# Kernel optimization log

Hardware: AMD Instinct MI355X
Metric: run time of the kernel (lower is better)

## Reference

```python
import jax, jax.numpy as jnp
import numpy as np

NUM_HEADS = 16
HEAD_DIM = 64


def setup_inputs() -> dict:
    key = jax.random.key(0)
    k1, k2, k3 = jax.random.split(key, 3)
    B, N, D = 4, 2048, NUM_HEADS * HEAD_DIM
    q = jax.random.normal(k1, (B, N, D), dtype=jnp.float32)
    k = jax.random.normal(k2, (B, N, D), dtype=jnp.float32)
    v = jax.random.normal(k3, (B, N, D), dtype=jnp.float32)
    # causal mask: True where attention is allowed
    attn_mask = jnp.tril(jnp.ones((N, N), dtype=bool))
    return {"q": q, "k": k, "v": v, "attn_mask": attn_mask}


def reference(q, k, v, attn_mask):
    B, N, D = q.shape
    H, Hd = NUM_HEADS, HEAD_DIM
    # [B, N, H*Hd] -> [B, H, N, Hd]
    qh = q.reshape(B, N, H, Hd).transpose(0, 2, 1, 3)
    kh = k.reshape(B, N, H, Hd).transpose(0, 2, 1, 3)
    vh = v.reshape(B, N, H, Hd).transpose(0, 2, 1, 3)
    scale = 1.0 / jnp.sqrt(jnp.asarray(Hd, dtype=q.dtype))
    scores = jnp.einsum('bhqd,bhkd->bhqk', qh, kh) * scale  # [B,H,N,N]
    scores = jnp.where(attn_mask[None, None, :, :], scores, -jnp.inf)
    probs = jax.nn.softmax(scores, axis=-1)
    y = jnp.einsum('bhqk,bhkd->bhqd', probs, vh)  # [B,H,N,Hd]
    return y.transpose(0, 2, 1, 3).reshape(B, N, H * Hd)
```

## Files before the change

### kernel.cpp

```cpp
#include <hip/hip_runtime.h>

#define RS 1024
#define SEQLEN 2048

typedef __fp16 f16;
typedef __attribute__((ext_vector_type(2))) __fp16 half2v;
typedef __attribute__((ext_vector_type(4))) __fp16 half4v;
typedef __attribute__((ext_vector_type(8))) __fp16 half8v;
typedef __attribute__((ext_vector_type(4))) float float4v;

__device__ __forceinline__ half8v pack8h(float4v a, float4v b) {
  union { half8v v; half2v h[4]; } u;
  u.h[0] = __builtin_amdgcn_cvt_pkrtz(a[0], a[1]);
  u.h[1] = __builtin_amdgcn_cvt_pkrtz(a[2], a[3]);
  u.h[2] = __builtin_amdgcn_cvt_pkrtz(b[0], b[1]);
  u.h[3] = __builtin_amdgcn_cvt_pkrtz(b[2], b[3]);
  return u.v;
}

template<bool DOMASK>
__device__ __forceinline__ void compute_tile(
    const f16* __restrict__ Klds, const f16* __restrict__ VB,
    const half8v (&aq)[2], float4v (&o)[4], float& lp,
    int quad, int lm, int wlm)
{
  float4v sfr[4];
  #pragma unroll
  for (int nb = 0; nb < 4; ++nb) sfr[nb] = (float4v){0.f, 0.f, 0.f, 0.f};

  __builtin_amdgcn_s_setprio(1);
  #pragma unroll
  for (int nb = 0; nb < 4; ++nb) {
    const int row = nb*16 + lm;
    #pragma unroll
    for (int s = 0; s < 2; ++s) {
      const half8v ak = *(const half8v*)&Klds[row*64 + (((s*4 + quad) ^ (lm & 7)) * 8)];
      sfr[nb] = __builtin_amdgcn_mfma_f32_16x16x32_f16(ak, aq[s], sfr[nb], 0, 0, 0);
    }
  }
  __builtin_amdgcn_s_setprio(0);

  half4v pa[4];
  float acc = 0.f;
  #pragma unroll
  for (int nb = 0; nb < 4; ++nb) {
    float p[4];
    #pragma unroll
    for (int r = 0; r < 4; ++r) {
      const int n = nb*16 + quad*4 + r;
      const float e = __builtin_amdgcn_exp2f(sfr[nb][r]);
      p[r] = (DOMASK && (n > wlm)) ? 0.f : e;
    }
    acc += (p[0] + p[1]) + (p[2] + p[3]);
    union { half4v v; half2v h[2]; } u;
    u.h[0] = __builtin_amdgcn_cvt_pkrtz(p[0], p[1]);
    u.h[1] = __builtin_amdgcn_cvt_pkrtz(p[2], p[3]);
    pa[nb] = u.v;
  }
  lp += acc;

  __builtin_amdgcn_s_setprio(1);
  #pragma unroll
  for (int nb = 0; nb < 4; ++nb) {
    const int kvq = nb*4 + quad;
    #pragma unroll
    for (int db = 0; db < 4; ++db) {
      const half4v vb = *(const half4v*)&VB[kvq*256 + (((db*16 + lm) ^ quad) * 4)];
      o[db] = __builtin_amdgcn_mfma_f32_16x16x16f16(pa[nb], vb, o[db], 0, 0, 0);
    }
  }
  __builtin_amdgcn_s_setprio(0);
}

__global__ __launch_bounds__(512, 4) void fa_fwd(
    const float* __restrict__ Qg, const float* __restrict__ Kg,
    const float* __restrict__ Vg, float* __restrict__ Og)
{
  __shared__ __align__(16) f16 Klds[2][64*64];
  __shared__ __align__(16) f16 VB[2][64*64];

  const int tid  = threadIdx.x;
  const int w    = tid >> 6;
  const int lane = tid & 63;
  const int quad = lane >> 4;
  const int lm   = lane & 15;
  const int wlm  = (w & 3)*16 + lm;

  const int bid = blockIdx.x;
  const int bh  = bid & 63;
  const int st  = 15 - (bid >> 6);
  const int j1  = 2*st + 1;
  const int j1w = 2*st + (w >> 2);

  const size_t headoff = (size_t)(bh >> 4) * SEQLEN * RS + (size_t)(bh & 15) * 64;
  const float* Kb = Kg + headoff;
  const float* Vb = Vg + headoff;

  const float qs = 0.18033688011112042f;
  half8v aq[2];
  {
    const float* qp = Qg + headoff + (size_t)(st*128 + w*16 + lm) * RS + quad*8;
    aq[0] = pack8h(*(const float4v*)qp * qs,        *(const float4v*)(qp + 4) * qs);
    aq[1] = pack8h(*(const float4v*)(qp + 32) * qs, *(const float4v*)(qp + 36) * qs);
  }

  float4v o[4] = {};
  float lp = 0.f;

  const bool doK = (tid >= 256);
  const int kr   = tid & 255;
  const int krow = kr >> 3, kcb = kr & 7;
  const int rgrp = kr >> 4, dgrp = kr & 15;
  const int r3 = rgrp & 3;

  float4v pr[4];
  auto loadKV = [&](int kv0) {
    if (doK) {
      const float* kp = Kb + (size_t)(kv0 + krow) * RS + kcb*8;
      pr[0] = *(const float4v*)kp;       pr[1] = *(const float4v*)(kp + 4);
      const float* kp2 = kp + (size_t)32 * RS;
      pr[2] = *(const float4v*)kp2;      pr[3] = *(const float4v*)(kp2 + 4);
    } else {
      const float* vp = Vb + (size_t)(kv0 + rgrp*4) * RS + dgrp*4;
      pr[0] = *(const float4v*)vp;
      pr[1] = *(const float4v*)(vp + RS);
      pr[2] = *(const float4v*)(vp + 2*RS);
      pr[3] = *(const float4v*)(vp + 3*RS);
    }
  };
  auto stageKV = [&](f16* Kd, f16* Vd) {
    if (doK) {
      *(half8v*)&Kd[krow*64 + ((kcb ^ (krow & 7)) * 8)] = pack8h(pr[0], pr[1]);
      const int row2 = krow + 32;
      *(half8v*)&Kd[row2*64 + ((kcb ^ (row2 & 7)) * 8)] = pack8h(pr[2], pr[3]);
    } else {
      union { half8v v8[2]; half2v h[8]; } u;
      #pragma unroll
      for (int cp = 0; cp < 4; ++cp) {
        const int c = cp ^ r3;
        u.h[cp*2]     = __builtin_amdgcn_cvt_pkrtz(pr[0][c], pr[1][c]);
        u.h[cp*2 + 1] = __builtin_amdgcn_cvt_pkrtz(pr[2][c], pr[3][c]);
      }
      f16* dst = &Vd[rgrp*256 + dgrp*16];
      *(half8v*)dst       = u.v8[0];
      *(half8v*)(dst + 8) = u.v8[1];
    }
  };

  loadKV(0);
  stageKV(Klds[0], VB[0]);
  loadKV(64);
  __syncthreads();

  for (int j = 0; j <= j1; ++j) {
    const int cur = j & 1;
    if (j < j1) {
      stageKV(Klds[cur ^ 1], VB[cur ^ 1]);
      if (j + 1 < j1) loadKV((j + 2) * 64);
    }
    if (j <= j1w) {
      if (j < j1w)
        compute_tile<false>(Klds[cur], VB[cur], aq, o, lp, quad, lm, wlm);
      else
        compute_tile<true >(Klds[cur], VB[cur], aq, o, lp, quad, lm, wlm);
    }
    __syncthreads();
  }

  float l = lp;
  l += __shfl_xor(l, 16);
  l += __shfl_xor(l, 32);
  const float linv = 1.0f / l;
  #pragma unroll
  for (int r = 0; r < 4; ++r) {
    const float nrm = __shfl(linv, quad*4 + r);
    float* op = Og + headoff + (size_t)(st*128 + w*16 + quad*4 + r) * RS;
    #pragma unroll
    for (int db = 0; db < 4; ++db)
      op[db*16 + lm] = o[db][r] * nrm;
  }
}

extern "C" void kernel_launch(void* const* d_in, const int* in_sizes, int n_in,
                              void* d_out, int out_size, void* d_ws, size_t ws_size,
                              hipStream_t stream) {
  const float* q = (const float*)d_in[0];
  const float* k = (const float*)d_in[1];
  const float* v = (const float*)d_in[2];
  float* out = (float*)d_out;
  fa_fwd<<<dim3(16 * 64), dim3(512), 0, stream>>>(q, k, v, out);
}
```

Measured before the change: 181.4 us.

## Widen V LDS reads to 8 halves and reorder causal tile scheduling

The V tile in shared memory is re-laid out with an XOR swizzle so each lane reads 8 halves at once and feeds two MFMAs, halving the number of LDS read instructions in the PV product. The staging side now writes four 4-half chunks instead of two 8-half chunks. Block-to-query-tile mapping changes from strictly heaviest-first to a zigzag ordering (15..12, 8..11, 7..4, 0..3) to spread causal work across waves of blocks. The new schedule may hurt tail balance compared with longest-first ordering.

New measurement: 178.8 us. No clear change (-1.4%).

```diff
diff --git a/kernel.cpp b/kernel.cpp
--- a/kernel.cpp
+++ b/kernel.cpp
@@ -61,12 +61,14 @@
 
   __builtin_amdgcn_s_setprio(1);
   #pragma unroll
-  for (int nb = 0; nb < 4; ++nb) {
-    const int kvq = nb*4 + quad;
+  for (int e = 0; e < 2; ++e) {
     #pragma unroll
-    for (int db = 0; db < 4; ++db) {
-      const half4v vb = *(const half4v*)&VB[kvq*256 + (((db*16 + lm) ^ quad) * 4)];
-      o[db] = __builtin_amdgcn_mfma_f32_16x16x16f16(pa[nb], vb, o[db], 0, 0, 0);
+    for (int nb = 0; nb < 4; ++nb) {
+      const int kvq = nb*4 + quad;
+      union { half8v v; half4v h[2]; } uu;
+      uu.v = *(const half8v*)&VB[kvq*256 + (((e*16 + lm) ^ kvq) * 8)];
+      o[2*e]     = __builtin_amdgcn_mfma_f32_16x16x16f16(pa[nb], uu.h[0], o[2*e],     0, 0, 0);
+      o[2*e + 1] = __builtin_amdgcn_mfma_f32_16x16x16f16(pa[nb], uu.h[1], o[2*e + 1], 0, 0, 0);
     }
   }
   __builtin_amdgcn_s_setprio(0);
@@ -88,7 +90,9 @@
 
   const int bid = blockIdx.x;
   const int bh  = bid & 63;
-  const int st  = 15 - (bid >> 6);
+  const int g   = (bid >> 6) & 3;
+  const int s   = bid >> 8;
+  const int st  = (s == 0) ? 15 - g : (s == 1) ? 8 + g : (s == 2) ? 7 - g : g;
   const int j1  = 2*st + 1;
   const int j1w = 2*st + (w >> 2);
 
@@ -111,7 +115,9 @@
   const int kr   = tid & 255;
   const int krow = kr >> 3, kcb = kr & 7;
   const int rgrp = kr >> 4, dgrp = kr & 15;
-  const int r3 = rgrp & 3;
+  const int ve   = dgrp >> 3;
+  const int vv   = (dgrp >> 2) & 1;
+  const int lmb  = (dgrp & 3) * 4;
 
   float4v pr[4];
   auto loadKV = [&](int kv0) {
@@ -134,16 +140,14 @@
       const int row2 = krow + 32;
       *(half8v*)&Kd[row2*64 + ((kcb ^ (row2 & 7)) * 8)] = pack8h(pr[2], pr[3]);
     } else {
-      union { half8v v8[2]; half2v h[8]; } u;
       #pragma unroll
-      for (int cp = 0; cp < 4; ++cp) {
-        const int c = cp ^ r3;
-        u.h[cp*2]     = __builtin_amdgcn_cvt_pkrtz(pr[0][c], pr[1][c]);
-        u.h[cp*2 + 1] = __builtin_amdgcn_cvt_pkrtz(pr[2][c], pr[3][c]);
+      for (int cc = 0; cc < 4; ++cc) {
+        union { half4v v; half2v h[2]; } u;
+        u.h[0] = __builtin_amdgcn_cvt_pkrtz(pr[0][cc], pr[1][cc]);
+        u.h[1] = __builtin_amdgcn_cvt_pkrtz(pr[2][cc], pr[3][cc]);
+        const int lmv = lmb + cc;
+        *(half4v*)&Vd[rgrp*256 + (((ve*16 + lmv) ^ rgrp) * 8) + vv*4] = u.v;
       }
-      f16* dst = &Vd[rgrp*256 + dgrp*16];
-      *(half8v*)dst       = u.v8[0];
-      *(half8v*)(dst + 8) = u.v8[1];
     }
   };
 
```
